# Performance work log

Measured on AMD Instinct MI355X. Metric: run time of the kernel, lower is better.

Reference implementation:

```python
import jax, jax.numpy as jnp
import numpy as np

N = 50000      # nodes
E = 800000     # edges (avg degree 16)
DIN = 128
DH = 128
DOUT = 40
ALPHA = 0.1
BETA = 1.0


def gcn_conv(x, src, dst, ew, W, b, n):
    """PyG GCNConv: add self-loops, symmetric deg^-1/2 normalization, gather-scatter."""
    idx = jnp.arange(n)
    s = jnp.concatenate([src, idx])
    d = jnp.concatenate([dst, idx])
    w = jnp.concatenate([ew, jnp.ones((n,), x.dtype)])
    deg = jax.ops.segment_sum(w, d, num_segments=n)            # [N]
    dinv = jnp.where(deg > 0, jax.lax.rsqrt(deg), 0.0)
    norm = dinv[s] * w * dinv[d]                               # [E+N]
    h = x @ W                                                  # [N, dout]
    msg = h[s] * norm[:, None]                                 # gather + scale
    out = jax.ops.segment_sum(msg, d, num_segments=n)          # scatter-add
    return out + b


def setup_inputs() -> dict:
    key = jax.random.key(0)
    ks = jax.random.split(key, 10)
    x = jax.random.normal(ks[0], (N, DIN), jnp.float32)
    edge_index = jax.random.randint(ks[1], (2, E), 0, N, dtype=jnp.int64)
    edge_weight = jax.random.uniform(ks[2], (E,), jnp.float32)
    W1 = jax.random.normal(ks[3], (DIN, DH), jnp.float32) / np.float32(np.sqrt(DIN))
    b1 = jnp.zeros((DH,), jnp.float32)
    W2 = jax.random.normal(ks[4], (DH, DH), jnp.float32) / np.float32(np.sqrt(DH))
    b2 = jnp.zeros((DH,), jnp.float32)
    W3 = jax.random.normal(ks[5], (DH, DOUT), jnp.float32) / np.float32(np.sqrt(DH))
    b3 = jnp.zeros((DOUT,), jnp.float32)
    return {"x": x, "edge_index": edge_index, "edge_weight": edge_weight,
            "W1": W1, "b1": b1, "W2": W2, "b2": b2, "W3": W3, "b3": b3}


def reference(x, edge_index, edge_weight, W1, b1, W2, b2, W3, b3):
    src, dst = edge_index[0], edge_index[1]
    ones_w = jnp.ones((E,), x.dtype)
    h1 = jax.nn.relu(gcn_conv(x, src, dst, ones_w, W1, b1, N))   # conv1 (edge_weight=None)
    hc = gcn_conv(h1, src, dst, edge_weight, W2, b2, N)          # crf_layer with edge_weight
    h = ALPHA * h1 + BETA * hc                                   # weighted residual combo
    # LearnableBernoulliDropout: identity in eval mode
    out = gcn_conv(h, src, dst, ones_w, W3, b3, N)               # conv2
    return jax.nn.log_softmax(out, axis=1)
```

## Files before the change

kernel.cpp:

```cpp
#include <hip/hip_runtime.h>
#include <math.h>

#define DIN  128
#define DH   128
#define DOUT 40
#define ALPHA_C 0.1f
#define BETA_C  1.0f
#define SLOT 64

typedef __attribute__((ext_vector_type(8))) short short8;
typedef __attribute__((ext_vector_type(4))) float floatx4;

static inline int cdiv_h(int a, int b) { return (a + b - 1) / b; }

static __device__ __forceinline__ unsigned short f2b(float f) {
    unsigned u = __float_as_uint(f);
    u = u + 0x7FFFu + ((u >> 16) & 1u);
    return (unsigned short)(u >> 16);
}
static __device__ __forceinline__ unsigned pk2(float x, float y) {
    return (unsigned)f2b(x) | ((unsigned)f2b(y) << 16);
}
static __device__ __forceinline__ float2 b2f2(unsigned u) {
    float2 r;
    r.x = __uint_as_float(u << 16);
    r.y = __uint_as_float(u & 0xFFFF0000u);
    return r;
}

__global__ __launch_bounds__(256) void build_slots(const int* __restrict__ src,
                                                   const int* __restrict__ dst,
                                                   const float* __restrict__ ew,
                                                   int* cnt,
                                                   int2* __restrict__ csr, int E) {
    int half = (E + 1) >> 1;
    int e = blockIdx.x * 256 + threadIdx.x;
    if (e >= half) return;
    {
        int d = dst[e];
        int pos = atomicAdd(&cnt[d], 1);
        if (pos < SLOT) { int2 r; r.x = src[e]; r.y = __float_as_int(ew[e]); csr[(d << 6) + pos] = r; }
    }
    int e2 = e + half;
    if (e2 < E) {
        int d = dst[e2];
        int pos = atomicAdd(&cnt[d], 1);
        if (pos < SLOT) { int2 r; r.x = src[e2]; r.y = __float_as_int(ew[e2]); csr[(d << 6) + pos] = r; }
    }
}

__global__ __launch_bounds__(256) void wdeg_dinv(const int* __restrict__ cnt,
                                                 const int2* __restrict__ csr,
                                                 float* __restrict__ dinv1,
                                                 float* __restrict__ dinv2, int n) {
    int i = blockIdx.x * 256 + threadIdx.x;
    if (i >= n) return;
    int c = cnt[i]; if (c > SLOT) c = SLOT;
    dinv1[i] = rsqrtf((float)c + 1.f);
    float s = 1.f;
    int jb = i << 6;
    for (int j = 0; j < c; ++j) s += __int_as_float(csr[jb + j].y);
    dinv2[i] = rsqrtf(s);
}

template <bool ABF16>
__global__ __launch_bounds__(256) void gemm128(const void* __restrict__ Ain,
                                               const float* __restrict__ W,
                                               unsigned short* __restrict__ C, int M) {
    __shared__ short As[128 * 128];
    __shared__ short Bs[128 * 128];
    int t = threadIdx.x;
    int blockM = blockIdx.x * 128;

    {
        int r = t >> 1, h = t & 1;
        int rg = blockM + r; if (rg > M - 1) rg = M - 1;
        if (ABF16) {
            const uint4* arow = (const uint4*)((const unsigned short*)Ain + (size_t)rg * 128);
            #pragma unroll
            for (int i = 0; i < 8; ++i) {
                int chunk = h * 8 + i;
                uint4 v = arow[chunk];
                *(uint4*)&As[r * 128 + ((chunk ^ (r & 7)) * 8)] = v;
            }
        } else {
            const float4* arow = (const float4*)((const float*)Ain + (size_t)rg * 128);
            #pragma unroll
            for (int i = 0; i < 8; ++i) {
                int chunk = h * 8 + i;
                float4 v0 = arow[chunk * 2], v1 = arow[chunk * 2 + 1];
                uint4 p;
                p.x = pk2(v0.x, v0.y); p.y = pk2(v0.z, v0.w);
                p.z = pk2(v1.x, v1.y); p.w = pk2(v1.z, v1.w);
                *(uint4*)&As[r * 128 + ((chunk ^ (r & 7)) * 8)] = p;
            }
        }
    }
    {
        int n = t & 127;
        int k0 = (t >> 7) * 64;
        #pragma unroll
        for (int it = 0; it < 8; ++it) {
            int k = k0 + it * 8;
            float f0 = W[(size_t)(k + 0) * 128 + n];
            float f1 = W[(size_t)(k + 1) * 128 + n];
            float f2 = W[(size_t)(k + 2) * 128 + n];
            float f3 = W[(size_t)(k + 3) * 128 + n];
            float f4 = W[(size_t)(k + 4) * 128 + n];
            float f5 = W[(size_t)(k + 5) * 128 + n];
            float f6 = W[(size_t)(k + 6) * 128 + n];
            float f7 = W[(size_t)(k + 7) * 128 + n];
            uint4 p;
            p.x = pk2(f0, f1); p.y = pk2(f2, f3);
            p.z = pk2(f4, f5); p.w = pk2(f6, f7);
            *(uint4*)&Bs[n * 128 + (((k >> 3) ^ (n & 7)) * 8)] = p;
        }
    }
    __syncthreads();

    int w = t >> 6, l = t & 63;
    int q = l >> 4, lm = l & 15;
    int rowoff = (w >> 1) * 64, coloff = (w & 1) * 64;

    floatx4 acc[4][4] = {};
    #pragma unroll
    for (int ks = 0; ks < 4; ++ks) {
        int chunk = ks * 4 + q;
        int sw = (chunk ^ (lm & 7)) * 8;
        short8 af[4], bf[4];
        #pragma unroll
        for (int tm = 0; tm < 4; ++tm)
            af[tm] = *(const short8*)&As[(rowoff + tm * 16 + lm) * 128 + sw];
        #pragma unroll
        for (int tn = 0; tn < 4; ++tn)
            bf[tn] = *(const short8*)&Bs[(coloff + tn * 16 + lm) * 128 + sw];
        #pragma unroll
        for (int tm = 0; tm < 4; ++tm)
            #pragma unroll
            for (int tn = 0; tn < 4; ++tn)
                acc[tm][tn] = __builtin_amdgcn_mfma_f32_16x16x32_bf16(af[tm], bf[tn], acc[tm][tn], 0, 0, 0);
    }

    #pragma unroll
    for (int tm = 0; tm < 4; ++tm) {
        #pragma unroll
        for (int reg = 0; reg < 4; ++reg) {
            int row = blockM + rowoff + tm * 16 + q * 4 + reg;
            if (row >= M) continue;
            #pragma unroll
            for (int tn = 0; tn < 4; ++tn) {
                int col = coloff + tn * 16 + lm;
                C[(size_t)row * 128 + col] = f2b(acc[tm][tn][reg]);
            }
        }
    }
}

__global__ __launch_bounds__(256) void gemm40_lsm(const unsigned short* __restrict__ Ain,
                                                  const float* __restrict__ W,
                                                  const float* __restrict__ bias,
                                                  float* __restrict__ out, int M) {
    __shared__ short As[128 * 128];
    __shared__ short Bs[48 * 128];
    int t = threadIdx.x;
    int blockM = blockIdx.x * 128;

    {
        int r = t >> 1, h = t & 1;
        int rg = blockM + r; if (rg > M - 1) rg = M - 1;
        const uint4* arow = (const uint4*)(Ain + (size_t)rg * 128);
        #pragma unroll
        for (int i = 0; i < 8; ++i) {
            int chunk = h * 8 + i;
            uint4 v = arow[chunk];
            *(uint4*)&As[r * 128 + ((chunk ^ (r & 7)) * 8)] = v;
        }
    }
    {
        int n = t & 63;
        int k0 = (t >> 6) * 32;
        #pragma unroll
        for (int it = 0; it < 4; ++it) {
            int k = k0 + it * 8;
            uint4 p = {0, 0, 0, 0};
            if (n < 40) {
                float f0 = W[(size_t)(k + 0) * 40 + n];
                float f1 = W[(size_t)(k + 1) * 40 + n];
                float f2 = W[(size_t)(k + 2) * 40 + n];
                float f3 = W[(size_t)(k + 3) * 40 + n];
                float f4 = W[(size_t)(k + 4) * 40 + n];
                float f5 = W[(size_t)(k + 5) * 40 + n];
                float f6 = W[(size_t)(k + 6) * 40 + n];
                float f7 = W[(size_t)(k + 7) * 40 + n];
                p.x = pk2(f0, f1); p.y = pk2(f2, f3);
                p.z = pk2(f4, f5); p.w = pk2(f6, f7);
            }
            if (n < 48)
                *(uint4*)&Bs[n * 128 + (((k >> 3) ^ (n & 7)) * 8)] = p;
        }
    }
    __syncthreads();

    int w = t >> 6, l = t & 63;
    int q = l >> 4, lm = l & 15;
    int rowoff = w * 32;

    floatx4 acc[2][3] = {};
    #pragma unroll
    for (int ks = 0; ks < 4; ++ks) {
        int chunk = ks * 4 + q;
        int sw = (chunk ^ (lm & 7)) * 8;
        short8 af[2], bf[3];
        #pragma unroll
        for (int tm = 0; tm < 2; ++tm)
            af[tm] = *(const short8*)&As[(rowoff + tm * 16 + lm) * 128 + sw];
        #pragma unroll
        for (int tn = 0; tn < 3; ++tn)
            bf[tn] = *(const short8*)&Bs[(tn * 16 + lm) * 128 + sw];
        #pragma unroll
        for (int tm = 0; tm < 2; ++tm)
            #pragma unroll
            for (int tn = 0; tn < 3; ++tn)
                acc[tm][tn] = __builtin_amdgcn_mfma_f32_16x16x32_bf16(af[tm], bf[tn], acc[tm][tn], 0, 0, 0);
    }

    float bb0 = bias[lm];
    float bb1 = bias[16 + lm];
    float bb2 = (lm < 8) ? bias[32 + lm] : 0.f;
    #pragma unroll
    for (int tm = 0; tm < 2; ++tm) {
        #pragma unroll
        for (int reg = 0; reg < 4; ++reg) {
            int row = blockM + rowoff + tm * 16 + q * 4 + reg;
            float v0 = acc[tm][0][reg] + bb0;
            float v1 = acc[tm][1][reg] + bb1;
            float v2 = (lm < 8) ? acc[tm][2][reg] + bb2 : -INFINITY;
            float mx = fmaxf(fmaxf(v0, v1), v2);
            #pragma unroll
            for (int o = 1; o < 16; o <<= 1) mx = fmaxf(mx, __shfl_xor(mx, o, 64));
            float ss = expf(v0 - mx) + expf(v1 - mx) + ((lm < 8) ? expf(v2 - mx) : 0.f);
            #pragma unroll
            for (int o = 1; o < 16; o <<= 1) ss += __shfl_xor(ss, o, 64);
            float ls = mx + logf(ss);
            if (row < M) {
                out[(size_t)row * 40 + lm]      = v0 - ls;
                out[(size_t)row * 40 + 16 + lm] = v1 - ls;
                if (lm < 8) out[(size_t)row * 40 + 32 + lm] = v2 - ls;
            }
        }
    }
}

template <int MODE>
__global__ __launch_bounds__(256) void agg128(const unsigned short* __restrict__ hpre,
                                              unsigned short* __restrict__ io,
                                              const float* __restrict__ bias,
                                              const float* __restrict__ dinv,
                                              const int* __restrict__ cnt,
                                              const int2* __restrict__ csr, int n) {
    int row = blockIdx.x * 4 + (threadIdx.x >> 6);
    if (row >= n) return;
    int lane = threadIdx.x & 63;
    int q = lane >> 4, m = lane & 15;
    const uint4* hp4 = (const uint4*)hpre;

    float di = dinv[row];
    float acc[8] = {};

    int c = cnt[row]; if (c > SLOT) c = SLOT;
    int jb = row << 6;
    int je = jb + c;

    int j = jb + q;
    #define ACC8(V, CC) { \
        float2 p0 = b2f2(V.x), p1 = b2f2(V.y), p2 = b2f2(V.z), p3 = b2f2(V.w); \
        acc[0] = fmaf(CC, p0.x, acc[0]); acc[1] = fmaf(CC, p0.y, acc[1]); \
        acc[2] = fmaf(CC, p1.x, acc[2]); acc[3] = fmaf(CC, p1.y, acc[3]); \
        acc[4] = fmaf(CC, p2.x, acc[4]); acc[5] = fmaf(CC, p2.y, acc[5]); \
        acc[6] = fmaf(CC, p3.x, acc[6]); acc[7] = fmaf(CC, p3.y, acc[7]); }

    for (; j + 4 < je; j += 8) {
        int2 e0 = csr[j];
        int2 e1 = csr[j + 4];
        uint4 v0 = hp4[(size_t)e0.x * 16 + m];
        uint4 v1 = hp4[(size_t)e1.x * 16 + m];
        float c0 = (MODE == 1) ? dinv[e0.x] * __int_as_float(e0.y) * di : dinv[e0.x] * di;
        float c1 = (MODE == 1) ? dinv[e1.x] * __int_as_float(e1.y) * di : dinv[e1.x] * di;
        ACC8(v0, c0);
        ACC8(v1, c1);
    }
    if (j < je) {
        int2 e0 = csr[j];
        uint4 v0 = hp4[(size_t)e0.x * 16 + m];
        float c0 = (MODE == 1) ? dinv[e0.x] * __int_as_float(e0.y) * di : dinv[e0.x] * di;
        ACC8(v0, c0);
    }
    #undef ACC8

    #pragma unroll
    for (int k = 0; k < 8; ++k) {
        acc[k] += __shfl_xor(acc[k], 16, 64);
        acc[k] += __shfl_xor(acc[k], 32, 64);
    }

    if (q == 0) {
        float d2 = di * di;
        uint4 self = hp4[(size_t)row * 16 + m];
        float2 s0 = b2f2(self.x), s1 = b2f2(self.y), s2 = b2f2(self.z), s3 = b2f2(self.w);
        float v[8] = { fmaf(s0.x, d2, acc[0]), fmaf(s0.y, d2, acc[1]),
                       fmaf(s1.x, d2, acc[2]), fmaf(s1.y, d2, acc[3]),
                       fmaf(s2.x, d2, acc[4]), fmaf(s2.y, d2, acc[5]),
                       fmaf(s3.x, d2, acc[6]), fmaf(s3.y, d2, acc[7]) };
        uint4* iop = (uint4*)io + (size_t)row * 16 + m;
        if (MODE != 2) {
            float4 ba = ((const float4*)bias)[m * 2];
            float4 bbv = ((const float4*)bias)[m * 2 + 1];
            v[0] += ba.x; v[1] += ba.y; v[2] += ba.z; v[3] += ba.w;
            v[4] += bbv.x; v[5] += bbv.y; v[6] += bbv.z; v[7] += bbv.w;
        }
        if (MODE == 0) {
            #pragma unroll
            for (int k = 0; k < 8; ++k) v[k] = fmaxf(v[k], 0.f);
        } else if (MODE == 1) {
            uint4 h1 = *iop;
            float2 a0 = b2f2(h1.x), a1 = b2f2(h1.y), a2 = b2f2(h1.z), a3 = b2f2(h1.w);
            v[0] = fmaf(ALPHA_C, a0.x, BETA_C * v[0]); v[1] = fmaf(ALPHA_C, a0.y, BETA_C * v[1]);
            v[2] = fmaf(ALPHA_C, a1.x, BETA_C * v[2]); v[3] = fmaf(ALPHA_C, a1.y, BETA_C * v[3]);
            v[4] = fmaf(ALPHA_C, a2.x, BETA_C * v[4]); v[5] = fmaf(ALPHA_C, a2.y, BETA_C * v[5]);
            v[6] = fmaf(ALPHA_C, a3.x, BETA_C * v[6]); v[7] = fmaf(ALPHA_C, a3.y, BETA_C * v[7]);
        }
        uint4 o;
        o.x = pk2(v[0], v[1]); o.y = pk2(v[2], v[3]);
        o.z = pk2(v[4], v[5]); o.w = pk2(v[6], v[7]);
        *iop = o;
    }
}

extern "C" void kernel_launch(void* const* d_in, const int* in_sizes, int n_in,
                              void* d_out, int out_size, void* d_ws, size_t ws_size,
                              hipStream_t stream) {
    const float* x   = (const float*)d_in[0];
    const int*   ei  = (const int*)  d_in[1];
    const float* ew  = (const float*)d_in[2];
    const float* W1  = (const float*)d_in[3];
    const float* b1  = (const float*)d_in[4];
    const float* W2  = (const float*)d_in[5];
    const float* b2  = (const float*)d_in[6];
    const float* W3  = (const float*)d_in[7];
    const float* b3  = (const float*)d_in[8];
    float* out = (float*)d_out;

    const int Nn = in_sizes[0] / DIN;
    const int E  = in_sizes[1] / 2;
    const int* src = ei;
    const int* dst = ei + E;

    char* wsb = (char*)d_ws;
    int*   cnt   = (int*)wsb;                            wsb += (size_t)Nn * 4;
    float* dinv1 = (float*)wsb;                          wsb += (size_t)Nn * 4;
    float* dinv2 = (float*)wsb;                          wsb += (size_t)Nn * 4;
    int2*  csr   = (int2*)wsb;                           wsb += (size_t)Nn * SLOT * 8;
    unsigned short* hpreb = (unsigned short*)wsb;        wsb += (size_t)Nn * DH * 2;
    unsigned short* h1b   = (unsigned short*)wsb;        wsb += (size_t)Nn * DH * 2;

    hipMemsetAsync(cnt, 0, (size_t)Nn * 4, stream);
    build_slots<<<cdiv_h((E + 1) / 2, 256), 256, 0, stream>>>(src, dst, ew, cnt, csr, E);
    wdeg_dinv<<<cdiv_h(Nn, 256), 256, 0, stream>>>(cnt, csr, dinv1, dinv2, Nn);

    int gemmGrid = cdiv_h(Nn, 128);
    int aggGrid = cdiv_h(Nn, 4);

    gemm128<false><<<gemmGrid, 256, 0, stream>>>(x, W1, hpreb, Nn);
    agg128<0><<<aggGrid, 256, 0, stream>>>(hpreb, h1b, b1, dinv1, cnt, csr, Nn);

    gemm128<true><<<gemmGrid, 256, 0, stream>>>(h1b, W2, hpreb, Nn);
    agg128<1><<<aggGrid, 256, 0, stream>>>(hpreb, h1b, b2, dinv2, cnt, csr, Nn);

    agg128<2><<<aggGrid, 256, 0, stream>>>(h1b, hpreb, b3, dinv1, cnt, csr, Nn);
    gemm40_lsm<<<gemmGrid, 256, 0, stream>>>(hpreb, W3, b3, out, Nn);
}
```

Baseline: 295.0 us.

## Partition edge slot lists per XCD with workgroup-scope atomics and 8-way aggregation

Graph construction now keeps a separate counter array and a 16-slot bucket per destination node for each of the 8 XCDs, chosen from the hardware XCC id. Slot positions come from relaxed workgroup-scope atomics, which is meant to avoid cross-XCD contention on one shared counter. A pack kernel folds the per-XCD counts into a nibble word per node and computes both degree normalizations. Aggregation is rewritten so that 8 groups of 8 lanes each walk one XCD partition and load 32 bytes per lane. In exchange the CSR is twice as large and sparser, the counter memset is 8x bigger, each XCD bucket is capped at 15 edges, and correctness relies on the workgroup-scope atomics behaving as device-coherent within one XCD.

```diff
diff --git a/kernel.cpp b/kernel.cpp
--- a/kernel.cpp
+++ b/kernel.cpp
@@ -6,7 +6,8 @@
 #define DOUT 40
 #define ALPHA_C 0.1f
 #define BETA_C  1.0f
-#define SLOT 64
+#define NXCD 8
+#define PSLOT 16
 
 typedef __attribute__((ext_vector_type(8))) short short8;
 typedef __attribute__((ext_vector_type(4))) float floatx4;
@@ -28,39 +29,57 @@
     return r;
 }
 
-__global__ __launch_bounds__(256) void build_slots(const int* __restrict__ src,
-                                                   const int* __restrict__ dst,
-                                                   const float* __restrict__ ew,
-                                                   int* cnt,
-                                                   int2* __restrict__ csr, int E) {
-    int half = (E + 1) >> 1;
-    int e = blockIdx.x * 256 + threadIdx.x;
-    if (e >= half) return;
-    {
-        int d = dst[e];
-        int pos = atomicAdd(&cnt[d], 1);
-        if (pos < SLOT) { int2 r; r.x = src[e]; r.y = __float_as_int(ew[e]); csr[(d << 6) + pos] = r; }
-    }
-    int e2 = e + half;
-    if (e2 < E) {
-        int d = dst[e2];
-        int pos = atomicAdd(&cnt[d], 1);
-        if (pos < SLOT) { int2 r; r.x = src[e2]; r.y = __float_as_int(ew[e2]); csr[(d << 6) + pos] = r; }
-    }
-}
-
-__global__ __launch_bounds__(256) void wdeg_dinv(const int* __restrict__ cnt,
+__global__ __launch_bounds__(256) void build_part(const int* __restrict__ src,
+                                                  const int* __restrict__ dst,
+                                                  const float* __restrict__ ew,
+                                                  int* __restrict__ cnt8,
+                                                  int2* __restrict__ csr, int N, int E) {
+    unsigned xcc = __builtin_amdgcn_s_getreg((31u << 11) | 20u) & 7u;
+    int quarter = (E + 3) >> 2;
+    int e0 = blockIdx.x * 256 + threadIdx.x;
+    int* cntp = cnt8 + (size_t)xcc * N;
+
+    int idx[4]; int d[4], s[4]; float w[4]; int pos[4]; bool v[4];
+    #pragma unroll
+    for (int k = 0; k < 4; ++k) { idx[k] = e0 + k * quarter; v[k] = idx[k] < E; }
+    #pragma unroll
+    for (int k = 0; k < 4; ++k) if (v[k]) { d[k] = dst[idx[k]]; s[k] = src[idx[k]]; w[k] = ew[idx[k]]; }
+    #pragma unroll
+    for (int k = 0; k < 4; ++k) if (v[k])
+        pos[k] = __hip_atomic_fetch_add(&cntp[d[k]], 1, __ATOMIC_RELAXED, __HIP_MEMORY_SCOPE_WORKGROUP);
+    #pragma unroll
+    for (int k = 0; k < 4; ++k) if (v[k] && pos[k] < PSLOT - 1) {
+        int2 r; r.x = s[k]; r.y = __float_as_int(w[k]);
+        csr[((size_t)d[k] << 7) + (xcc << 4) + pos[k]] = r;
+    }
+}
+
+__global__ __launch_bounds__(256) void pack_dinv(const int* __restrict__ cnt8,
                                                  const int2* __restrict__ csr,
+                                                 unsigned* __restrict__ nibs,
                                                  float* __restrict__ dinv1,
-                                                 float* __restrict__ dinv2, int n) {
+                                                 float* __restrict__ dinv2, int N) {
     int i = blockIdx.x * 256 + threadIdx.x;
-    if (i >= n) return;
-    int c = cnt[i]; if (c > SLOT) c = SLOT;
-    dinv1[i] = rsqrtf((float)c + 1.f);
-    float s = 1.f;
-    int jb = i << 6;
-    for (int j = 0; j < c; ++j) s += __int_as_float(csr[jb + j].y);
-    dinv2[i] = rsqrtf(s);
+    if (i >= N) return;
+    unsigned nib = 0;
+    int tot = 0;
+    int cx[NXCD];
+    #pragma unroll
+    for (int x = 0; x < NXCD; ++x) {
+        int c = cnt8[(size_t)x * N + i];
+        if (c > PSLOT - 1) c = PSLOT - 1;
+        cx[x] = c; tot += c;
+        nib |= (unsigned)c << (4 * x);
+    }
+    float sw = 1.f;
+    #pragma unroll
+    for (int x = 0; x < NXCD; ++x) {
+        size_t jb = ((size_t)i << 7) + (x << 4);
+        for (int j = 0; j < cx[x]; ++j) sw += __int_as_float(csr[jb + j].y);
+    }
+    nibs[i] = nib;
+    dinv1[i] = rsqrtf((float)tot + 1.f);
+    dinv2[i] = rsqrtf(sw);
 }
 
 template <bool ABF16>
@@ -252,87 +271,108 @@
 }
 
 template <int MODE>
-__global__ __launch_bounds__(256) void agg128(const unsigned short* __restrict__ hpre,
-                                              unsigned short* __restrict__ io,
-                                              const float* __restrict__ bias,
-                                              const float* __restrict__ dinv,
-                                              const int* __restrict__ cnt,
-                                              const int2* __restrict__ csr, int n) {
+__global__ __launch_bounds__(256) void agg128p(const unsigned short* __restrict__ hpre,
+                                               unsigned short* __restrict__ io,
+                                               const float* __restrict__ bias,
+                                               const float* __restrict__ dinv,
+                                               const unsigned* __restrict__ nibs,
+                                               const int2* __restrict__ csr, int n) {
     int row = blockIdx.x * 4 + (threadIdx.x >> 6);
     if (row >= n) return;
     int lane = threadIdx.x & 63;
-    int q = lane >> 4, m = lane & 15;
+    int g = lane >> 3, i = lane & 7;
     const uint4* hp4 = (const uint4*)hpre;
 
     float di = dinv[row];
-    float acc[8] = {};
-
-    int c = cnt[row]; if (c > SLOT) c = SLOT;
-    int jb = row << 6;
-    int je = jb + c;
-
-    int j = jb + q;
-    #define ACC8(V, CC) { \
-        float2 p0 = b2f2(V.x), p1 = b2f2(V.y), p2 = b2f2(V.z), p3 = b2f2(V.w); \
-        acc[0] = fmaf(CC, p0.x, acc[0]); acc[1] = fmaf(CC, p0.y, acc[1]); \
-        acc[2] = fmaf(CC, p1.x, acc[2]); acc[3] = fmaf(CC, p1.y, acc[3]); \
-        acc[4] = fmaf(CC, p2.x, acc[4]); acc[5] = fmaf(CC, p2.y, acc[5]); \
-        acc[6] = fmaf(CC, p3.x, acc[6]); acc[7] = fmaf(CC, p3.y, acc[7]); }
-
-    for (; j + 4 < je; j += 8) {
-        int2 e0 = csr[j];
-        int2 e1 = csr[j + 4];
-        uint4 v0 = hp4[(size_t)e0.x * 16 + m];
-        uint4 v1 = hp4[(size_t)e1.x * 16 + m];
+    int c = (int)((nibs[row] >> (4 * g)) & 15u);
+    size_t jb = ((size_t)row << 7) + (g << 4);
+
+    float acc[16] = {};
+    #define ACC16(VA, VB, CC) { float2 p; \
+        p = b2f2(VA.x); acc[0]  = fmaf(CC, p.x, acc[0]);  acc[1]  = fmaf(CC, p.y, acc[1]); \
+        p = b2f2(VA.y); acc[2]  = fmaf(CC, p.x, acc[2]);  acc[3]  = fmaf(CC, p.y, acc[3]); \
+        p = b2f2(VA.z); acc[4]  = fmaf(CC, p.x, acc[4]);  acc[5]  = fmaf(CC, p.y, acc[5]); \
+        p = b2f2(VA.w); acc[6]  = fmaf(CC, p.x, acc[6]);  acc[7]  = fmaf(CC, p.y, acc[7]); \
+        p = b2f2(VB.x); acc[8]  = fmaf(CC, p.x, acc[8]);  acc[9]  = fmaf(CC, p.y, acc[9]); \
+        p = b2f2(VB.y); acc[10] = fmaf(CC, p.x, acc[10]); acc[11] = fmaf(CC, p.y, acc[11]); \
+        p = b2f2(VB.z); acc[12] = fmaf(CC, p.x, acc[12]); acc[13] = fmaf(CC, p.y, acc[13]); \
+        p = b2f2(VB.w); acc[14] = fmaf(CC, p.x, acc[14]); acc[15] = fmaf(CC, p.y, acc[15]); }
+
+    int j = 0;
+    for (; j + 1 < c; j += 2) {
+        int2 e0 = csr[jb + j], e1 = csr[jb + j + 1];
+        uint4 va0 = hp4[(size_t)e0.x * 16 + i * 2];
+        uint4 vb0 = hp4[(size_t)e0.x * 16 + i * 2 + 1];
+        uint4 va1 = hp4[(size_t)e1.x * 16 + i * 2];
+        uint4 vb1 = hp4[(size_t)e1.x * 16 + i * 2 + 1];
         float c0 = (MODE == 1) ? dinv[e0.x] * __int_as_float(e0.y) * di : dinv[e0.x] * di;
         float c1 = (MODE == 1) ? dinv[e1.x] * __int_as_float(e1.y) * di : dinv[e1.x] * di;
-        ACC8(v0, c0);
-        ACC8(v1, c1);
-    }
-    if (j < je) {
-        int2 e0 = csr[j];
-        uint4 v0 = hp4[(size_t)e0.x * 16 + m];
+        ACC16(va0, vb0, c0);
+        ACC16(va1, vb1, c1);
+    }
+    if (j < c) {
+        int2 e0 = csr[jb + j];
+        uint4 va0 = hp4[(size_t)e0.x * 16 + i * 2];
+        uint4 vb0 = hp4[(size_t)e0.x * 16 + i * 2 + 1];
         float c0 = (MODE == 1) ? dinv[e0.x] * __int_as_float(e0.y) * di : dinv[e0.x] * di;
-        ACC8(v0, c0);
-    }
-    #undef ACC8
-
-    #pragma unroll
-    for (int k = 0; k < 8; ++k) {
+        ACC16(va0, vb0, c0);
+    }
+    #undef ACC16
+
+    #pragma unroll
+    for (int k = 0; k < 16; ++k) {
+        acc[k] += __shfl_xor(acc[k], 8, 64);
         acc[k] += __shfl_xor(acc[k], 16, 64);
         acc[k] += __shfl_xor(acc[k], 32, 64);
     }
 
-    if (q == 0) {
+    if (g == 0) {
         float d2 = di * di;
-        uint4 self = hp4[(size_t)row * 16 + m];
-        float2 s0 = b2f2(self.x), s1 = b2f2(self.y), s2 = b2f2(self.z), s3 = b2f2(self.w);
-        float v[8] = { fmaf(s0.x, d2, acc[0]), fmaf(s0.y, d2, acc[1]),
-                       fmaf(s1.x, d2, acc[2]), fmaf(s1.y, d2, acc[3]),
-                       fmaf(s2.x, d2, acc[4]), fmaf(s2.y, d2, acc[5]),
-                       fmaf(s3.x, d2, acc[6]), fmaf(s3.y, d2, acc[7]) };
-        uint4* iop = (uint4*)io + (size_t)row * 16 + m;
+        uint4 sa = hp4[(size_t)row * 16 + i * 2];
+        uint4 sb = hp4[(size_t)row * 16 + i * 2 + 1];
+        float v[16];
+        {
+            float2 p;
+            p = b2f2(sa.x); v[0]  = fmaf(p.x, d2, acc[0]);  v[1]  = fmaf(p.y, d2, acc[1]);
+            p = b2f2(sa.y); v[2]  = fmaf(p.x, d2, acc[2]);  v[3]  = fmaf(p.y, d2, acc[3]);
+            p = b2f2(sa.z); v[4]  = fmaf(p.x, d2, acc[4]);  v[5]  = fmaf(p.y, d2, acc[5]);
+            p = b2f2(sa.w); v[6]  = fmaf(p.x, d2, acc[6]);  v[7]  = fmaf(p.y, d2, acc[7]);
+            p = b2f2(sb.x); v[8]  = fmaf(p.x, d2, acc[8]);  v[9]  = fmaf(p.y, d2, acc[9]);
+            p = b2f2(sb.y); v[10] = fmaf(p.x, d2, acc[10]); v[11] = fmaf(p.y, d2, acc[11]);
+            p = b2f2(sb.z); v[12] = fmaf(p.x, d2, acc[12]); v[13] = fmaf(p.y, d2, acc[13]);
+            p = b2f2(sb.w); v[14] = fmaf(p.x, d2, acc[14]); v[15] = fmaf(p.y, d2, acc[15]);
+        }
         if (MODE != 2) {
-            float4 ba = ((const float4*)bias)[m * 2];
-            float4 bbv = ((const float4*)bias)[m * 2 + 1];
-            v[0] += ba.x; v[1] += ba.y; v[2] += ba.z; v[3] += ba.w;
-            v[4] += bbv.x; v[5] += bbv.y; v[6] += bbv.z; v[7] += bbv.w;
-        }
+            const float4* b4 = (const float4*)bias;
+            #pragma unroll
+            for (int k = 0; k < 4; ++k) {
+                float4 bb = b4[i * 4 + k];
+                v[k * 4 + 0] += bb.x; v[k * 4 + 1] += bb.y;
+                v[k * 4 + 2] += bb.z; v[k * 4 + 3] += bb.w;
+            }
+        }
+        uint4* iop = (uint4*)io + (size_t)row * 16 + i * 2;
         if (MODE == 0) {
             #pragma unroll
-            for (int k = 0; k < 8; ++k) v[k] = fmaxf(v[k], 0.f);
+            for (int k = 0; k < 16; ++k) v[k] = fmaxf(v[k], 0.f);
         } else if (MODE == 1) {
-            uint4 h1 = *iop;
-            float2 a0 = b2f2(h1.x), a1 = b2f2(h1.y), a2 = b2f2(h1.z), a3 = b2f2(h1.w);
-            v[0] = fmaf(ALPHA_C, a0.x, BETA_C * v[0]); v[1] = fmaf(ALPHA_C, a0.y, BETA_C * v[1]);
-            v[2] = fmaf(ALPHA_C, a1.x, BETA_C * v[2]); v[3] = fmaf(ALPHA_C, a1.y, BETA_C * v[3]);
-            v[4] = fmaf(ALPHA_C, a2.x, BETA_C * v[4]); v[5] = fmaf(ALPHA_C, a2.y, BETA_C * v[5]);
-            v[6] = fmaf(ALPHA_C, a3.x, BETA_C * v[6]); v[7] = fmaf(ALPHA_C, a3.y, BETA_C * v[7]);
-        }
-        uint4 o;
-        o.x = pk2(v[0], v[1]); o.y = pk2(v[2], v[3]);
-        o.z = pk2(v[4], v[5]); o.w = pk2(v[6], v[7]);
-        *iop = o;
+            uint4 h1a = iop[0], h1b = iop[1];
+            float2 p;
+            p = b2f2(h1a.x); v[0]  = fmaf(ALPHA_C, p.x, BETA_C * v[0]);  v[1]  = fmaf(ALPHA_C, p.y, BETA_C * v[1]);
+            p = b2f2(h1a.y); v[2]  = fmaf(ALPHA_C, p.x, BETA_C * v[2]);  v[3]  = fmaf(ALPHA_C, p.y, BETA_C * v[3]);
+            p = b2f2(h1a.z); v[4]  = fmaf(ALPHA_C, p.x, BETA_C * v[4]);  v[5]  = fmaf(ALPHA_C, p.y, BETA_C * v[5]);
+            p = b2f2(h1a.w); v[6]  = fmaf(ALPHA_C, p.x, BETA_C * v[6]);  v[7]  = fmaf(ALPHA_C, p.y, BETA_C * v[7]);
+            p = b2f2(h1b.x); v[8]  = fmaf(ALPHA_C, p.x, BETA_C * v[8]);  v[9]  = fmaf(ALPHA_C, p.y, BETA_C * v[9]);
+            p = b2f2(h1b.y); v[10] = fmaf(ALPHA_C, p.x, BETA_C * v[10]); v[11] = fmaf(ALPHA_C, p.y, BETA_C * v[11]);
+            p = b2f2(h1b.z); v[12] = fmaf(ALPHA_C, p.x, BETA_C * v[12]); v[13] = fmaf(ALPHA_C, p.y, BETA_C * v[13]);
+            p = b2f2(h1b.w); v[14] = fmaf(ALPHA_C, p.x, BETA_C * v[14]); v[15] = fmaf(ALPHA_C, p.y, BETA_C * v[15]);
+        }
+        uint4 oa, ob;
+        oa.x = pk2(v[0], v[1]);   oa.y = pk2(v[2], v[3]);
+        oa.z = pk2(v[4], v[5]);   oa.w = pk2(v[6], v[7]);
+        ob.x = pk2(v[8], v[9]);   ob.y = pk2(v[10], v[11]);
+        ob.z = pk2(v[12], v[13]); ob.w = pk2(v[14], v[15]);
+        iop[0] = oa; iop[1] = ob;
     }
 }
 
@@ -356,26 +396,27 @@
     const int* dst = ei + E;
 
     char* wsb = (char*)d_ws;
-    int*   cnt   = (int*)wsb;                            wsb += (size_t)Nn * 4;
-    float* dinv1 = (float*)wsb;                          wsb += (size_t)Nn * 4;
-    float* dinv2 = (float*)wsb;                          wsb += (size_t)Nn * 4;
-    int2*  csr   = (int2*)wsb;                           wsb += (size_t)Nn * SLOT * 8;
+    int*      cnt8  = (int*)wsb;                         wsb += (size_t)NXCD * Nn * 4;
+    unsigned* nibs  = (unsigned*)wsb;                    wsb += (size_t)Nn * 4;
+    float*    dinv1 = (float*)wsb;                       wsb += (size_t)Nn * 4;
+    float*    dinv2 = (float*)wsb;                       wsb += (size_t)Nn * 4;
+    int2*     csr   = (int2*)wsb;                        wsb += (size_t)Nn * NXCD * PSLOT * 8;
     unsigned short* hpreb = (unsigned short*)wsb;        wsb += (size_t)Nn * DH * 2;
     unsigned short* h1b   = (unsigned short*)wsb;        wsb += (size_t)Nn * DH * 2;
 
-    hipMemsetAsync(cnt, 0, (size_t)Nn * 4, stream);
-    build_slots<<<cdiv_h((E + 1) / 2, 256), 256, 0, stream>>>(src, dst, ew, cnt, csr, E);
-    wdeg_dinv<<<cdiv_h(Nn, 256), 256, 0, stream>>>(cnt, csr, dinv1, dinv2, Nn);
+    hipMemsetAsync(cnt8, 0, (size_t)NXCD * Nn * 4, stream);
+    build_part<<<cdiv_h((E + 3) / 4, 256), 256, 0, stream>>>(src, dst, ew, cnt8, csr, Nn, E);
+    pack_dinv<<<cdiv_h(Nn, 256), 256, 0, stream>>>(cnt8, csr, nibs, dinv1, dinv2, Nn);
 
     int gemmGrid = cdiv_h(Nn, 128);
     int aggGrid = cdiv_h(Nn, 4);
 
     gemm128<false><<<gemmGrid, 256, 0, stream>>>(x, W1, hpreb, Nn);
-    agg128<0><<<aggGrid, 256, 0, stream>>>(hpreb, h1b, b1, dinv1, cnt, csr, Nn);
+    agg128p<0><<<aggGrid, 256, 0, stream>>>(hpreb, h1b, b1, dinv1, nibs, csr, Nn);
 
     gemm128<true><<<gemmGrid, 256, 0, stream>>>(h1b, W2, hpreb, Nn);
-    agg128<1><<<aggGrid, 256, 0, stream>>>(hpreb, h1b, b2, dinv2, cnt, csr, Nn);
-
-    agg128<2><<<aggGrid, 256, 0, stream>>>(h1b, hpreb, b3, dinv1, cnt, csr, Nn);
+    agg128p<1><<<aggGrid, 256, 0, stream>>>(hpreb, h1b, b2, dinv2, nibs, csr, Nn);
+
+    agg128p<2><<<aggGrid, 256, 0, stream>>>(h1b, hpreb, b3, dinv1, nibs, csr, Nn);
     gemm40_lsm<<<gemmGrid, 256, 0, stream>>>(hpreb, W3, b3, out, Nn);
 }
```

Result: slower. 319.7 us (+8.4%).
